# Optimization experiments

Hardware: AMD Instinct MI355X
Metric: run time of the kernel (lower is better)

The kernel has to match this reference:

```python
import math
import jax, jax.numpy as jnp
import numpy as np

B, S, H, D = 2, 2048, 16, 128
NEG = -1000000000.0  # same finite mask value as the original blockwise code


def setup_inputs() -> dict:
    key = jax.random.key(0)
    kq, kk, kv = jax.random.split(key, 3)
    query = jax.random.normal(kq, (B, S, H, D), dtype=jnp.float32)
    key_t = jax.random.normal(kk, (B, S, H, D), dtype=jnp.float32)
    value = jax.random.normal(kv, (B, S, H, D), dtype=jnp.float32)
    return {"query": query, "key": key_t, "value": value}


def reference(query, key, value):
    # RingAttention.__call__ with use_ring_attention=True, causal=True, no req.
    # ring_attention's blockwise online-softmax is mathematically identical to
    # standard softmax attention when S is a multiple of the block sizes (no
    # padding), with masked logits set to -1e9 (which underflows to exactly 0
    # after exp in fp32, matching the explicit *mask in the original).
    scale = 1.0 / math.sqrt(query.shape[-1])
    q = jnp.transpose(query, (0, 2, 1, 3)).astype(jnp.float32)  # [B,H,S,D]
    k = jnp.transpose(key, (0, 2, 1, 3)).astype(jnp.float32)
    v = jnp.transpose(value, (0, 2, 1, 3)).astype(jnp.float32)
    s = q.shape[2]
    scores = jnp.einsum('bhqd,bhkd->bhqk', q, k) * scale  # [B,H,S,S]
    causal_mask = jnp.arange(s)[None, :] <= jnp.arange(s)[:, None]  # k <= q
    scores = jnp.where(causal_mask[None, None], scores, NEG)
    weights = jax.nn.softmax(scores, axis=-1)
    out = jnp.einsum('bhqk,bhkd->bhqd', weights, v)
    return jnp.transpose(out, (0, 2, 1, 3)).astype(query.dtype)  # [B,S,H,D]
```

## Files before the change

kernel.cpp:

```cpp
#include <hip/hip_runtime.h>
#include <hip/hip_bf16.h>

namespace {
constexpr int NB = 2, NS = 2048, NH = 16, ND = 128;
constexpr int QB = 64, KB = 64;
constexpr int NQT = NS / QB;
constexpr int ROWSTRIDE = NH * ND;
constexpr float SCALE_LOG2E = 0.08838834764831843f * 1.4426950408889634f;

constexpr int K_OFF = 0;
constexpr int V_OFF = 16384;
constexpr int P_OFF = 32768;
constexpr int P_WSZ = 2304;
constexpr int SMEM_SZ = P_OFF + 4 * P_WSZ;
}

typedef __attribute__((ext_vector_type(4))) float f32x4;
typedef __attribute__((ext_vector_type(8))) short bf16x8;
typedef __attribute__((ext_vector_type(2))) unsigned int u32x2;

__device__ __forceinline__ unsigned short f2bf(float f) {
  union { __hip_bfloat16 h; unsigned short u; } cv;
  cv.h = __float2bfloat16(f);
  return cv.u;
}

__device__ __forceinline__ float bcast_row(const float v[4], int lane) {
  int q = lane & 15;
  int src = ((q >> 2) << 4) | q;
  float a0 = __shfl(v[0], src, 64);
  float a1 = __shfl(v[1], src, 64);
  float a2 = __shfl(v[2], src, 64);
  float a3 = __shfl(v[3], src, 64);
  int r = q & 3;
  return (r == 0) ? a0 : ((r == 1) ? a1 : ((r == 2) ? a2 : a3));
}

__global__ __launch_bounds__(256)
void fattn_fwd(const float* __restrict__ Q, const float* __restrict__ K,
               const float* __restrict__ V, float* __restrict__ O) {
  __shared__ __align__(16) char smem[SMEM_SZ];

  const int pid = blockIdx.x;
  const int h = blockIdx.y;
  const int b = blockIdx.z;
  const int t = threadIdx.x;
  const int w = t >> 6;
  const int lane = t & 63;
  const int g = lane >> 4;
  const int cc = lane & 15;

  const size_t bh = ((size_t)b * NS * NH + h) * (size_t)ND;

  char* Kl = smem + K_OFF;
  char* Vl = smem + V_OFF;
  char* Pl = smem + P_OFF + w * P_WSZ;

  for (int half = 0; half < 2; ++half) {
    const int qt = half ? (NQT - 1 - pid) : pid;

    bf16x8 qf[4];
    {
      const float* qp = Q + bh + (size_t)(qt * QB + w * 16 + cc) * ROWSTRIDE;
#pragma unroll
      for (int dc = 0; dc < 4; ++dc) {
        f32x4 v0 = *reinterpret_cast<const f32x4*>(qp + dc * 32 + 8 * g);
        f32x4 v1 = *reinterpret_cast<const f32x4*>(qp + dc * 32 + 8 * g + 4);
        bf16x8 f;
        f[0] = (short)f2bf(v0[0]); f[1] = (short)f2bf(v0[1]);
        f[2] = (short)f2bf(v0[2]); f[3] = (short)f2bf(v0[3]);
        f[4] = (short)f2bf(v1[0]); f[5] = (short)f2bf(v1[1]);
        f[6] = (short)f2bf(v1[2]); f[7] = (short)f2bf(v1[3]);
        qf[dc] = f;
      }
    }

    f32x4 oacc[8];
#pragma unroll
    for (int i = 0; i < 8; ++i) { oacc[i][0] = 0.f; oacc[i][1] = 0.f; oacc[i][2] = 0.f; oacc[i][3] = 0.f; }
    float m_run[4] = {-1e30f, -1e30f, -1e30f, -1e30f};
    float l_run[4] = {0.f, 0.f, 0.f, 0.f};

    for (int kt = 0; kt <= qt; ++kt) {
      const int kb = kt * KB;

      {
        f32x4 kreg[8];
#pragma unroll
        for (int jj = 0; jj < 8; ++jj) {
          int idx = jj * 256 + t;
          int r = idx >> 5;
          int c4 = idx & 31;
          kreg[jj] = *reinterpret_cast<const f32x4*>(K + bh + (size_t)(kb + r) * ROWSTRIDE + c4 * 4);
        }
#pragma unroll
        for (int jj = 0; jj < 8; ++jj) {
          int idx = jj * 256 + t;
          int r = idx >> 5;
          int c4 = idx & 31;
          unsigned int klo = (unsigned int)f2bf(kreg[jj][0]) | ((unsigned int)f2bf(kreg[jj][1]) << 16);
          unsigned int khi = (unsigned int)f2bf(kreg[jj][2]) | ((unsigned int)f2bf(kreg[jj][3]) << 16);
          int kbyte = (r * 256 + c4 * 8) ^ ((r & 7) << 4);
          u32x2 kk; kk[0] = klo; kk[1] = khi;
          *reinterpret_cast<u32x2*>(Kl + kbyte) = kk;
        }
      }
      {
        f32x4 vreg[2][4];
        const int c4 = t & 31;
#pragma unroll
        for (int it = 0; it < 2; ++it) {
          int r0 = ((t >> 5) + 8 * it) * 4;
          const float* vp = V + bh + (size_t)(kb + r0) * ROWSTRIDE + c4 * 4;
#pragma unroll
          for (int j = 0; j < 4; ++j)
            vreg[it][j] = *reinterpret_cast<const f32x4*>(vp + (size_t)j * ROWSTRIDE);
        }
#pragma unroll
        for (int it = 0; it < 2; ++it) {
          int r0 = ((t >> 5) + 8 * it) * 4;
#pragma unroll
          for (int j = 0; j < 4; ++j) {
            int d = 4 * c4 + j;
            unsigned int lo = (unsigned int)f2bf(vreg[it][0][j]) | ((unsigned int)f2bf(vreg[it][1][j]) << 16);
            unsigned int hi = (unsigned int)f2bf(vreg[it][2][j]) | ((unsigned int)f2bf(vreg[it][3][j]) << 16);
            int vbyte = (d * 128 + r0 * 2) ^ (((d >> 1) & 7) << 4);
            u32x2 pk; pk[0] = lo; pk[1] = hi;
            *reinterpret_cast<u32x2*>(Vl + vbyte) = pk;
          }
        }
      }
      __syncthreads();

      f32x4 s[4];
#pragma unroll
      for (int nt = 0; nt < 4; ++nt) { s[nt][0] = 0.f; s[nt][1] = 0.f; s[nt][2] = 0.f; s[nt][3] = 0.f; }
      __builtin_amdgcn_s_setprio(1);
#pragma unroll
      for (int nt = 0; nt < 4; ++nt) {
        int row = nt * 16 + cc;
#pragma unroll
        for (int dc = 0; dc < 4; ++dc) {
          int byte = (row * 256 + dc * 64 + g * 16) ^ ((row & 7) << 4);
          bf16x8 kf = *reinterpret_cast<const bf16x8*>(Kl + byte);
          s[nt] = __builtin_amdgcn_mfma_f32_16x16x32_bf16(qf[dc], kf, s[nt], 0, 0, 0);
        }
      }
      __builtin_amdgcn_s_setprio(0);

      if (kt == qt) {
#pragma unroll
        for (int nt = 0; nt < 4; ++nt)
#pragma unroll
          for (int r = 0; r < 4; ++r)
            if (nt * 16 + cc > w * 16 + g * 4 + r) s[nt][r] = -1e30f;
      }

      float tmax[4];
#pragma unroll
      for (int r = 0; r < 4; ++r)
        tmax[r] = fmaxf(fmaxf(s[0][r], s[1][r]), fmaxf(s[2][r], s[3][r]));
#pragma unroll
      for (int off = 1; off < 16; off <<= 1) {
#pragma unroll
        for (int r = 0; r < 4; ++r)
          tmax[r] = fmaxf(tmax[r], __shfl_xor(tmax[r], off, 64));
      }
      float alpha[4];
#pragma unroll
      for (int r = 0; r < 4; ++r) {
        float mn = fmaxf(m_run[r], tmax[r]);
        alpha[r] = exp2f((m_run[r] - mn) * SCALE_LOG2E);
        m_run[r] = mn;
      }
      float p[4][4];
      float psum[4] = {0.f, 0.f, 0.f, 0.f};
#pragma unroll
      for (int nt = 0; nt < 4; ++nt)
#pragma unroll
        for (int r = 0; r < 4; ++r) {
          float pv = exp2f((s[nt][r] - m_run[r]) * SCALE_LOG2E);
          p[nt][r] = pv;
          psum[r] += pv;
        }
#pragma unroll
      for (int r = 0; r < 4; ++r) l_run[r] = l_run[r] * alpha[r] + psum[r];

      float aq = bcast_row(alpha, lane);
#pragma unroll
      for (int mt = 0; mt < 8; ++mt) {
        oacc[mt][0] *= aq; oacc[mt][1] *= aq; oacc[mt][2] *= aq; oacc[mt][3] *= aq;
      }

#pragma unroll
      for (int nt = 0; nt < 4; ++nt)
#pragma unroll
        for (int r = 0; r < 4; ++r)
          *reinterpret_cast<unsigned short*>(Pl + (g * 4 + r) * 144 + (nt * 16 + cc) * 2) =
              f2bf(p[nt][r]);

      asm volatile("s_waitcnt lgkmcnt(0)" ::: "memory");
      __builtin_amdgcn_sched_barrier(0);

      __builtin_amdgcn_s_setprio(1);
#pragma unroll
      for (int kc = 0; kc < 2; ++kc) {
        bf16x8 pf = *reinterpret_cast<const bf16x8*>(Pl + cc * 144 + kc * 64 + g * 16);
#pragma unroll
        for (int mt = 0; mt < 8; ++mt) {
          int d = mt * 16 + cc;
          int byte = (d * 128 + kc * 64 + g * 16) ^ (((d >> 1) & 7) << 4);
          bf16x8 vf = *reinterpret_cast<const bf16x8*>(Vl + byte);
          oacc[mt] = __builtin_amdgcn_mfma_f32_16x16x32_bf16(vf, pf, oacc[mt], 0, 0, 0);
        }
      }
      __builtin_amdgcn_s_setprio(0);
      __syncthreads();
    }

#pragma unroll
    for (int off = 1; off < 16; off <<= 1) {
#pragma unroll
      for (int r = 0; r < 4; ++r)
        l_run[r] += __shfl_xor(l_run[r], off, 64);
    }
    float Lq = bcast_row(l_run, lane);
    float inv = 1.0f / Lq;

    float* op = O + bh + (size_t)(qt * QB + w * 16 + cc) * ROWSTRIDE;
#pragma unroll
    for (int mt = 0; mt < 8; ++mt)
#pragma unroll
      for (int r = 0; r < 4; ++r)
        op[mt * 16 + g * 4 + r] = oacc[mt][r] * inv;
  }
}

extern "C" void kernel_launch(void* const* d_in, const int* in_sizes, int n_in,
                              void* d_out, int out_size, void* d_ws, size_t ws_size,
                              hipStream_t stream) {
  const float* Q = (const float*)d_in[0];
  const float* K = (const float*)d_in[1];
  const float* V = (const float*)d_in[2];
  float* O = (float*)d_out;
  dim3 grid(NQT / 2, NH, NB);
  fattn_fwd<<<grid, dim3(256), 0, stream>>>(Q, K, V, O);
}
```

Measured before the change: 266.4 us.

## Prefetch next K/V tile into registers during compute and remap block order

The K and V global loads for the next tile are now issued right after the LDS barrier, so their latency overlaps the QK^T, softmax and PV work of the current tile. The staged registers are converted to bf16 and stored to LDS at the start of the next iteration. The grid is also flattened to 1D with a remapping that interleaves blocks across groups of 8, likely aimed at XCD placement and L2 locality. The cost is higher register pressure from holding 16 f32x4 prefetch registers, which may reduce occupancy.

Result: slower. 287.4 us (+7.9%).

```diff
diff --git a/kernel.cpp b/kernel.cpp
--- a/kernel.cpp
+++ b/kernel.cpp
@@ -41,9 +41,12 @@
                const float* __restrict__ V, float* __restrict__ O) {
   __shared__ __align__(16) char smem[SMEM_SZ];
 
-  const int pid = blockIdx.x;
-  const int h = blockIdx.y;
-  const int b = blockIdx.z;
+  const int bid = blockIdx.x;
+  const int lid = (bid & 7) * 64 + (bid >> 3);
+  const int pid = lid & 15;
+  const int h = (lid >> 4) & 15;
+  const int b = lid >> 8;
+
   const int t = threadIdx.x;
   const int w = t >> 6;
   const int lane = t & 63;
@@ -55,6 +58,28 @@
   char* Kl = smem + K_OFF;
   char* Vl = smem + V_OFF;
   char* Pl = smem + P_OFF + w * P_WSZ;
+
+  f32x4 kpre[8];
+  f32x4 vpre[2][4];
+  const int kc4 = t & 31;
+  const int kr = t >> 5;
+  const int vr0a = (t >> 5) * 4;
+  const int vr0b = vr0a + 32;
+
+  auto issue_loads = [&](int kb) {
+#pragma unroll
+    for (int jj = 0; jj < 8; ++jj)
+      kpre[jj] = *reinterpret_cast<const f32x4*>(
+          K + bh + (size_t)(kb + kr + jj * 8) * ROWSTRIDE + kc4 * 4);
+#pragma unroll
+    for (int j = 0; j < 4; ++j)
+      vpre[0][j] = *reinterpret_cast<const f32x4*>(
+          V + bh + (size_t)(kb + vr0a + j) * ROWSTRIDE + kc4 * 4);
+#pragma unroll
+    for (int j = 0; j < 4; ++j)
+      vpre[1][j] = *reinterpret_cast<const f32x4*>(
+          V + bh + (size_t)(kb + vr0b + j) * ROWSTRIDE + kc4 * 4);
+  };
 
   for (int half = 0; half < 2; ++half) {
     const int qt = half ? (NQT - 1 - pid) : pid;
@@ -81,56 +106,34 @@
     float m_run[4] = {-1e30f, -1e30f, -1e30f, -1e30f};
     float l_run[4] = {0.f, 0.f, 0.f, 0.f};
 
+    issue_loads(0);
+
     for (int kt = 0; kt <= qt; ++kt) {
-      const int kb = kt * KB;
-
-      {
-        f32x4 kreg[8];
-#pragma unroll
-        for (int jj = 0; jj < 8; ++jj) {
-          int idx = jj * 256 + t;
-          int r = idx >> 5;
-          int c4 = idx & 31;
-          kreg[jj] = *reinterpret_cast<const f32x4*>(K + bh + (size_t)(kb + r) * ROWSTRIDE + c4 * 4);
-        }
-#pragma unroll
-        for (int jj = 0; jj < 8; ++jj) {
-          int idx = jj * 256 + t;
-          int r = idx >> 5;
-          int c4 = idx & 31;
-          unsigned int klo = (unsigned int)f2bf(kreg[jj][0]) | ((unsigned int)f2bf(kreg[jj][1]) << 16);
-          unsigned int khi = (unsigned int)f2bf(kreg[jj][2]) | ((unsigned int)f2bf(kreg[jj][3]) << 16);
-          int kbyte = (r * 256 + c4 * 8) ^ ((r & 7) << 4);
-          u32x2 kk; kk[0] = klo; kk[1] = khi;
-          *reinterpret_cast<u32x2*>(Kl + kbyte) = kk;
-        }
-      }
-      {
-        f32x4 vreg[2][4];
-        const int c4 = t & 31;
-#pragma unroll
-        for (int it = 0; it < 2; ++it) {
-          int r0 = ((t >> 5) + 8 * it) * 4;
-          const float* vp = V + bh + (size_t)(kb + r0) * ROWSTRIDE + c4 * 4;
-#pragma unroll
-          for (int j = 0; j < 4; ++j)
-            vreg[it][j] = *reinterpret_cast<const f32x4*>(vp + (size_t)j * ROWSTRIDE);
-        }
-#pragma unroll
-        for (int it = 0; it < 2; ++it) {
-          int r0 = ((t >> 5) + 8 * it) * 4;
-#pragma unroll
-          for (int j = 0; j < 4; ++j) {
-            int d = 4 * c4 + j;
-            unsigned int lo = (unsigned int)f2bf(vreg[it][0][j]) | ((unsigned int)f2bf(vreg[it][1][j]) << 16);
-            unsigned int hi = (unsigned int)f2bf(vreg[it][2][j]) | ((unsigned int)f2bf(vreg[it][3][j]) << 16);
-            int vbyte = (d * 128 + r0 * 2) ^ (((d >> 1) & 7) << 4);
-            u32x2 pk; pk[0] = lo; pk[1] = hi;
-            *reinterpret_cast<u32x2*>(Vl + vbyte) = pk;
-          }
+#pragma unroll
+      for (int jj = 0; jj < 8; ++jj) {
+        int r = kr + jj * 8;
+        unsigned int klo = (unsigned int)f2bf(kpre[jj][0]) | ((unsigned int)f2bf(kpre[jj][1]) << 16);
+        unsigned int khi = (unsigned int)f2bf(kpre[jj][2]) | ((unsigned int)f2bf(kpre[jj][3]) << 16);
+        int kbyte = (r * 256 + kc4 * 8) ^ ((r & 7) << 4);
+        u32x2 kk; kk[0] = klo; kk[1] = khi;
+        *reinterpret_cast<u32x2*>(Kl + kbyte) = kk;
+      }
+#pragma unroll
+      for (int it = 0; it < 2; ++it) {
+        int r0 = it ? vr0b : vr0a;
+#pragma unroll
+        for (int j = 0; j < 4; ++j) {
+          int d = 4 * kc4 + j;
+          unsigned int lo = (unsigned int)f2bf(vpre[it][0][j]) | ((unsigned int)f2bf(vpre[it][1][j]) << 16);
+          unsigned int hi = (unsigned int)f2bf(vpre[it][2][j]) | ((unsigned int)f2bf(vpre[it][3][j]) << 16);
+          int vbyte = (d * 128 + r0 * 2) ^ (((d >> 1) & 7) << 4);
+          u32x2 pk; pk[0] = lo; pk[1] = hi;
+          *reinterpret_cast<u32x2*>(Vl + vbyte) = pk;
         }
       }
       __syncthreads();
+
+      if (kt < qt) issue_loads((kt + 1) * KB);
 
       f32x4 s[4];
 #pragma unroll
@@ -243,6 +246,6 @@
   const float* K = (const float*)d_in[1];
   const float* V = (const float*)d_in[2];
   float* O = (float*)d_out;
-  dim3 grid(NQT / 2, NH, NB);
+  dim3 grid((NQT / 2) * NH * NB);
   fattn_fwd<<<grid, dim3(256), 0, stream>>>(Q, K, V, O);
 }
```

## Launch one query tile per block, longest-first with XCD-aware mapping, skip masked MFMAs

Applied to the files above, without the earlier changes.

The grid changes from 512 blocks that each process a paired short and long query tile to 1024 blocks that each process one tile. Blocks are ordered longest-first, and the flat block id is mapped so each (batch, head) pair stays on one XCD, which should improve L2 reuse of K and V. On the diagonal tile, QK^T and PV MFMAs for fully masked sub-tiles are skipped. The P LDS buffer now uses an XOR swizzle instead of padding, and launch bounds request 4 blocks per CU. The risks are losing the load balance that pairing gave, extra register pressure from the occupancy hint, and a dynamic register index for the diagonal mask.

After: 615.5 us. +131.0%, slower.

```diff
diff --git a/kernel.cpp b/kernel.cpp
--- a/kernel.cpp
+++ b/kernel.cpp
@@ -11,7 +11,7 @@
 constexpr int K_OFF = 0;
 constexpr int V_OFF = 16384;
 constexpr int P_OFF = 32768;
-constexpr int P_WSZ = 2304;
+constexpr int P_WSZ = 2048;
 constexpr int SMEM_SZ = P_OFF + 4 * P_WSZ;
 }
 
@@ -36,14 +36,19 @@
   return (r == 0) ? a0 : ((r == 1) ? a1 : ((r == 2) ? a2 : a3));
 }
 
-__global__ __launch_bounds__(256)
+__global__ __launch_bounds__(256, 4)
 void fattn_fwd(const float* __restrict__ Q, const float* __restrict__ K,
                const float* __restrict__ V, float* __restrict__ O) {
   __shared__ __align__(16) char smem[SMEM_SZ];
 
-  const int pid = blockIdx.x;
-  const int h = blockIdx.y;
-  const int b = blockIdx.z;
+  const int bid = blockIdx.x;
+  const int x = bid & 7;
+  const int j = bid >> 3;
+  const int qt = (NQT - 1) - (j >> 2);
+  const int hb = x + 8 * (j & 3);
+  const int h = hb >> 1;
+  const int b = hb & 1;
+
   const int t = threadIdx.x;
   const int w = t >> 6;
   const int lane = t & 63;
@@ -56,156 +61,160 @@
   char* Vl = smem + V_OFF;
   char* Pl = smem + P_OFF + w * P_WSZ;
 
-  for (int half = 0; half < 2; ++half) {
-    const int qt = half ? (NQT - 1 - pid) : pid;
-
-    bf16x8 qf[4];
+  const int kc4 = t & 31;
+  const int kr = t >> 5;
+  const int vr0a = (t >> 5) * 4;
+  const int vr0b = vr0a + 32;
+
+  bf16x8 qf[4];
+  {
+    const float* qp = Q + bh + (size_t)(qt * QB + w * 16 + cc) * ROWSTRIDE;
+#pragma unroll
+    for (int dc = 0; dc < 4; ++dc) {
+      f32x4 v0 = *reinterpret_cast<const f32x4*>(qp + dc * 32 + 8 * g);
+      f32x4 v1 = *reinterpret_cast<const f32x4*>(qp + dc * 32 + 8 * g + 4);
+      bf16x8 f;
+      f[0] = (short)f2bf(v0[0]); f[1] = (short)f2bf(v0[1]);
+      f[2] = (short)f2bf(v0[2]); f[3] = (short)f2bf(v0[3]);
+      f[4] = (short)f2bf(v1[0]); f[5] = (short)f2bf(v1[1]);
+      f[6] = (short)f2bf(v1[2]); f[7] = (short)f2bf(v1[3]);
+      qf[dc] = f;
+    }
+  }
+
+  f32x4 oacc[8];
+#pragma unroll
+  for (int i = 0; i < 8; ++i) { oacc[i][0] = 0.f; oacc[i][1] = 0.f; oacc[i][2] = 0.f; oacc[i][3] = 0.f; }
+  float m_run[4] = {-1e30f, -1e30f, -1e30f, -1e30f};
+  float l_run[4] = {0.f, 0.f, 0.f, 0.f};
+
+  for (int kt = 0; kt <= qt; ++kt) {
+    const int kb = kt * KB;
+    const bool diag = (kt == qt);
+
     {
-      const float* qp = Q + bh + (size_t)(qt * QB + w * 16 + cc) * ROWSTRIDE;
-#pragma unroll
-      for (int dc = 0; dc < 4; ++dc) {
-        f32x4 v0 = *reinterpret_cast<const f32x4*>(qp + dc * 32 + 8 * g);
-        f32x4 v1 = *reinterpret_cast<const f32x4*>(qp + dc * 32 + 8 * g + 4);
-        bf16x8 f;
-        f[0] = (short)f2bf(v0[0]); f[1] = (short)f2bf(v0[1]);
-        f[2] = (short)f2bf(v0[2]); f[3] = (short)f2bf(v0[3]);
-        f[4] = (short)f2bf(v1[0]); f[5] = (short)f2bf(v1[1]);
-        f[6] = (short)f2bf(v1[2]); f[7] = (short)f2bf(v1[3]);
-        qf[dc] = f;
-      }
-    }
-
-    f32x4 oacc[8];
-#pragma unroll
-    for (int i = 0; i < 8; ++i) { oacc[i][0] = 0.f; oacc[i][1] = 0.f; oacc[i][2] = 0.f; oacc[i][3] = 0.f; }
-    float m_run[4] = {-1e30f, -1e30f, -1e30f, -1e30f};
-    float l_run[4] = {0.f, 0.f, 0.f, 0.f};
-
-    for (int kt = 0; kt <= qt; ++kt) {
-      const int kb = kt * KB;
-
-      {
-        f32x4 kreg[8];
-#pragma unroll
-        for (int jj = 0; jj < 8; ++jj) {
-          int idx = jj * 256 + t;
-          int r = idx >> 5;
-          int c4 = idx & 31;
-          kreg[jj] = *reinterpret_cast<const f32x4*>(K + bh + (size_t)(kb + r) * ROWSTRIDE + c4 * 4);
+      f32x4 kreg[8];
+#pragma unroll
+      for (int jj = 0; jj < 8; ++jj)
+        kreg[jj] = *reinterpret_cast<const f32x4*>(
+            K + bh + (size_t)(kb + kr + jj * 8) * ROWSTRIDE + kc4 * 4);
+#pragma unroll
+      for (int jj = 0; jj < 8; ++jj) {
+        int r = kr + jj * 8;
+        unsigned int klo = (unsigned int)f2bf(kreg[jj][0]) | ((unsigned int)f2bf(kreg[jj][1]) << 16);
+        unsigned int khi = (unsigned int)f2bf(kreg[jj][2]) | ((unsigned int)f2bf(kreg[jj][3]) << 16);
+        int kbyte = (r * 256 + kc4 * 8) ^ ((r & 7) << 4);
+        u32x2 kk; kk[0] = klo; kk[1] = khi;
+        *reinterpret_cast<u32x2*>(Kl + kbyte) = kk;
+      }
+    }
+    {
+      f32x4 vreg[2][4];
+#pragma unroll
+      for (int it = 0; it < 2; ++it) {
+        int r0 = it ? vr0b : vr0a;
+        const float* vp = V + bh + (size_t)(kb + r0) * ROWSTRIDE + kc4 * 4;
+#pragma unroll
+        for (int jv = 0; jv < 4; ++jv)
+          vreg[it][jv] = *reinterpret_cast<const f32x4*>(vp + (size_t)jv * ROWSTRIDE);
+      }
+#pragma unroll
+      for (int it = 0; it < 2; ++it) {
+        int r0 = it ? vr0b : vr0a;
+#pragma unroll
+        for (int jv = 0; jv < 4; ++jv) {
+          int d = 4 * kc4 + jv;
+          unsigned int lo = (unsigned int)f2bf(vreg[it][0][jv]) | ((unsigned int)f2bf(vreg[it][1][jv]) << 16);
+          unsigned int hi = (unsigned int)f2bf(vreg[it][2][jv]) | ((unsigned int)f2bf(vreg[it][3][jv]) << 16);
+          int vbyte = (d * 128 + r0 * 2) ^ (((d >> 1) & 7) << 4);
+          u32x2 pk; pk[0] = lo; pk[1] = hi;
+          *reinterpret_cast<u32x2*>(Vl + vbyte) = pk;
         }
-#pragma unroll
-        for (int jj = 0; jj < 8; ++jj) {
-          int idx = jj * 256 + t;
-          int r = idx >> 5;
-          int c4 = idx & 31;
-          unsigned int klo = (unsigned int)f2bf(kreg[jj][0]) | ((unsigned int)f2bf(kreg[jj][1]) << 16);
-          unsigned int khi = (unsigned int)f2bf(kreg[jj][2]) | ((unsigned int)f2bf(kreg[jj][3]) << 16);
-          int kbyte = (r * 256 + c4 * 8) ^ ((r & 7) << 4);
-          u32x2 kk; kk[0] = klo; kk[1] = khi;
-          *reinterpret_cast<u32x2*>(Kl + kbyte) = kk;
-        }
-      }
-      {
-        f32x4 vreg[2][4];
-        const int c4 = t & 31;
-#pragma unroll
-        for (int it = 0; it < 2; ++it) {
-          int r0 = ((t >> 5) + 8 * it) * 4;
-          const float* vp = V + bh + (size_t)(kb + r0) * ROWSTRIDE + c4 * 4;
-#pragma unroll
-          for (int j = 0; j < 4; ++j)
-            vreg[it][j] = *reinterpret_cast<const f32x4*>(vp + (size_t)j * ROWSTRIDE);
-        }
-#pragma unroll
-        for (int it = 0; it < 2; ++it) {
-          int r0 = ((t >> 5) + 8 * it) * 4;
-#pragma unroll
-          for (int j = 0; j < 4; ++j) {
-            int d = 4 * c4 + j;
-            unsigned int lo = (unsigned int)f2bf(vreg[it][0][j]) | ((unsigned int)f2bf(vreg[it][1][j]) << 16);
-            unsigned int hi = (unsigned int)f2bf(vreg[it][2][j]) | ((unsigned int)f2bf(vreg[it][3][j]) << 16);
-            int vbyte = (d * 128 + r0 * 2) ^ (((d >> 1) & 7) << 4);
-            u32x2 pk; pk[0] = lo; pk[1] = hi;
-            *reinterpret_cast<u32x2*>(Vl + vbyte) = pk;
-          }
-        }
-      }
-      __syncthreads();
-
-      f32x4 s[4];
-#pragma unroll
-      for (int nt = 0; nt < 4; ++nt) { s[nt][0] = 0.f; s[nt][1] = 0.f; s[nt][2] = 0.f; s[nt][3] = 0.f; }
-      __builtin_amdgcn_s_setprio(1);
-#pragma unroll
-      for (int nt = 0; nt < 4; ++nt) {
+      }
+    }
+    __syncthreads();
+
+    f32x4 s[4];
+    __builtin_amdgcn_s_setprio(1);
+#pragma unroll
+    for (int nt = 0; nt < 4; ++nt) {
+      const bool active = !diag || (nt <= w);
+      if (active) {
+        f32x4 acc; acc[0] = 0.f; acc[1] = 0.f; acc[2] = 0.f; acc[3] = 0.f;
         int row = nt * 16 + cc;
 #pragma unroll
         for (int dc = 0; dc < 4; ++dc) {
           int byte = (row * 256 + dc * 64 + g * 16) ^ ((row & 7) << 4);
           bf16x8 kf = *reinterpret_cast<const bf16x8*>(Kl + byte);
-          s[nt] = __builtin_amdgcn_mfma_f32_16x16x32_bf16(qf[dc], kf, s[nt], 0, 0, 0);
+          acc = __builtin_amdgcn_mfma_f32_16x16x32_bf16(qf[dc], kf, acc, 0, 0, 0);
         }
-      }
-      __builtin_amdgcn_s_setprio(0);
-
-      if (kt == qt) {
-#pragma unroll
-        for (int nt = 0; nt < 4; ++nt)
-#pragma unroll
-          for (int r = 0; r < 4; ++r)
-            if (nt * 16 + cc > w * 16 + g * 4 + r) s[nt][r] = -1e30f;
-      }
-
-      float tmax[4];
+        s[nt] = acc;
+      } else {
+        s[nt][0] = -1e30f; s[nt][1] = -1e30f; s[nt][2] = -1e30f; s[nt][3] = -1e30f;
+      }
+    }
+    __builtin_amdgcn_s_setprio(0);
+
+    if (diag) {
 #pragma unroll
       for (int r = 0; r < 4; ++r)
-        tmax[r] = fmaxf(fmaxf(s[0][r], s[1][r]), fmaxf(s[2][r], s[3][r]));
-#pragma unroll
-      for (int off = 1; off < 16; off <<= 1) {
-#pragma unroll
-        for (int r = 0; r < 4; ++r)
-          tmax[r] = fmaxf(tmax[r], __shfl_xor(tmax[r], off, 64));
-      }
-      float alpha[4];
+        if (cc > g * 4 + r) s[w][r] = -1e30f;
+    }
+
+    float tmax[4];
+#pragma unroll
+    for (int r = 0; r < 4; ++r)
+      tmax[r] = fmaxf(fmaxf(s[0][r], s[1][r]), fmaxf(s[2][r], s[3][r]));
+#pragma unroll
+    for (int off = 1; off < 16; off <<= 1) {
+#pragma unroll
+      for (int r = 0; r < 4; ++r)
+        tmax[r] = fmaxf(tmax[r], __shfl_xor(tmax[r], off, 64));
+    }
+    float alpha[4];
+#pragma unroll
+    for (int r = 0; r < 4; ++r) {
+      float mn = fmaxf(m_run[r], tmax[r]);
+      alpha[r] = exp2f((m_run[r] - mn) * SCALE_LOG2E);
+      m_run[r] = mn;
+    }
+    float p[4][4];
+    float psum[4] = {0.f, 0.f, 0.f, 0.f};
+#pragma unroll
+    for (int nt = 0; nt < 4; ++nt)
 #pragma unroll
       for (int r = 0; r < 4; ++r) {
-        float mn = fmaxf(m_run[r], tmax[r]);
-        alpha[r] = exp2f((m_run[r] - mn) * SCALE_LOG2E);
-        m_run[r] = mn;
-      }
-      float p[4][4];
-      float psum[4] = {0.f, 0.f, 0.f, 0.f};
-#pragma unroll
-      for (int nt = 0; nt < 4; ++nt)
-#pragma unroll
-        for (int r = 0; r < 4; ++r) {
-          float pv = exp2f((s[nt][r] - m_run[r]) * SCALE_LOG2E);
-          p[nt][r] = pv;
-          psum[r] += pv;
-        }
-#pragma unroll
-      for (int r = 0; r < 4; ++r) l_run[r] = l_run[r] * alpha[r] + psum[r];
-
-      float aq = bcast_row(alpha, lane);
-#pragma unroll
-      for (int mt = 0; mt < 8; ++mt) {
-        oacc[mt][0] *= aq; oacc[mt][1] *= aq; oacc[mt][2] *= aq; oacc[mt][3] *= aq;
-      }
-
-#pragma unroll
-      for (int nt = 0; nt < 4; ++nt)
-#pragma unroll
-        for (int r = 0; r < 4; ++r)
-          *reinterpret_cast<unsigned short*>(Pl + (g * 4 + r) * 144 + (nt * 16 + cc) * 2) =
-              f2bf(p[nt][r]);
-
-      asm volatile("s_waitcnt lgkmcnt(0)" ::: "memory");
-      __builtin_amdgcn_sched_barrier(0);
-
-      __builtin_amdgcn_s_setprio(1);
-#pragma unroll
-      for (int kc = 0; kc < 2; ++kc) {
-        bf16x8 pf = *reinterpret_cast<const bf16x8*>(Pl + cc * 144 + kc * 64 + g * 16);
+        float pv = exp2f((s[nt][r] - m_run[r]) * SCALE_LOG2E);
+        p[nt][r] = pv;
+        psum[r] += pv;
+      }
+#pragma unroll
+    for (int r = 0; r < 4; ++r) l_run[r] = l_run[r] * alpha[r] + psum[r];
+
+    float aq = bcast_row(alpha, lane);
+#pragma unroll
+    for (int mt = 0; mt < 8; ++mt) {
+      oacc[mt][0] *= aq; oacc[mt][1] *= aq; oacc[mt][2] *= aq; oacc[mt][3] *= aq;
+    }
+
+#pragma unroll
+    for (int nt = 0; nt < 4; ++nt)
+#pragma unroll
+      for (int r = 0; r < 4; ++r) {
+        int pbyte = ((g * 4 + r) * 128 + (nt * 16 + cc) * 2) ^ (((g * 4 + r) & 7) << 4);
+        *reinterpret_cast<unsigned short*>(Pl + pbyte) = f2bf(p[nt][r]);
+      }
+
+    asm volatile("s_waitcnt lgkmcnt(0)" ::: "memory");
+    __builtin_amdgcn_sched_barrier(0);
+
+    __builtin_amdgcn_s_setprio(1);
+#pragma unroll
+    for (int kc = 0; kc < 2; ++kc) {
+      const bool active = !diag || (kc * 32 <= w * 16 + 15);
+      if (active) {
+        int pbyte = (cc * 128 + kc * 64 + g * 16) ^ ((cc & 7) << 4);
+        bf16x8 pf = *reinterpret_cast<const bf16x8*>(Pl + pbyte);
 #pragma unroll
         for (int mt = 0; mt < 8; ++mt) {
           int d = mt * 16 + cc;
@@ -214,26 +223,26 @@
           oacc[mt] = __builtin_amdgcn_mfma_f32_16x16x32_bf16(vf, pf, oacc[mt], 0, 0, 0);
         }
       }
-      __builtin_amdgcn_s_setprio(0);
-      __syncthreads();
-    }
-
-#pragma unroll
-    for (int off = 1; off < 16; off <<= 1) {
-#pragma unroll
-      for (int r = 0; r < 4; ++r)
-        l_run[r] += __shfl_xor(l_run[r], off, 64);
-    }
-    float Lq = bcast_row(l_run, lane);
-    float inv = 1.0f / Lq;
-
-    float* op = O + bh + (size_t)(qt * QB + w * 16 + cc) * ROWSTRIDE;
-#pragma unroll
-    for (int mt = 0; mt < 8; ++mt)
-#pragma unroll
-      for (int r = 0; r < 4; ++r)
-        op[mt * 16 + g * 4 + r] = oacc[mt][r] * inv;
+    }
+    __builtin_amdgcn_s_setprio(0);
+    __syncthreads();
   }
+
+#pragma unroll
+  for (int off = 1; off < 16; off <<= 1) {
+#pragma unroll
+    for (int r = 0; r < 4; ++r)
+      l_run[r] += __shfl_xor(l_run[r], off, 64);
+  }
+  float Lq = bcast_row(l_run, lane);
+  float inv = 1.0f / Lq;
+
+  float* op = O + bh + (size_t)(qt * QB + w * 16 + cc) * ROWSTRIDE;
+#pragma unroll
+  for (int mt = 0; mt < 8; ++mt)
+#pragma unroll
+    for (int r = 0; r < 4; ++r)
+      op[mt * 16 + g * 4 + r] = oacc[mt][r] * inv;
 }
 
 extern "C" void kernel_launch(void* const* d_in, const int* in_sizes, int n_in,
@@ -243,6 +252,6 @@
   const float* K = (const float*)d_in[1];
   const float* V = (const float*)d_in[2];
   float* O = (float*)d_out;
-  dim3 grid(NQT / 2, NH, NB);
+  dim3 grid(NQT * NH * NB);
   fattn_fwd<<<grid, dim3(256), 0, stream>>>(Q, K, V, O);
 }
```
